# Performance work log

Hardware: AMD Instinct MI355X
Metric: run time of the kernel (lower is better)

The kernel has to match this reference:

```python
import jax, jax.numpy as jnp
import numpy as np
import math

D_MODEL = 1024
N_HEAD = 16


def setup_inputs() -> dict:
    key = jax.random.key(0)
    ks = jax.random.split(key, 11)
    B, S, D = 2, 2048, D_MODEL
    s = 1.0 / math.sqrt(D)
    return {
        "q": jax.random.normal(ks[0], (B, S, D), dtype=jnp.float32),
        "k": jax.random.normal(ks[1], (B, S, D), dtype=jnp.float32),
        "v": jax.random.normal(ks[2], (B, S, D), dtype=jnp.float32),
        "w_q": jax.random.normal(ks[3], (D, D), dtype=jnp.float32) * s,
        "b_q": jnp.zeros((D,), dtype=jnp.float32),
        "w_k": jax.random.normal(ks[4], (D, D), dtype=jnp.float32) * s,
        "b_k": jnp.zeros((D,), dtype=jnp.float32),
        "w_v": jax.random.normal(ks[5], (D, D), dtype=jnp.float32) * s,
        "b_v": jnp.zeros((D,), dtype=jnp.float32),
        "w_out": jax.random.normal(ks[6], (D, D), dtype=jnp.float32) * s,
        "b_out": jnp.zeros((D,), dtype=jnp.float32),
    }


def _split_heads(x, n_head):
    B, S, D = x.shape
    return x.reshape(B, S, n_head, D // n_head).transpose(0, 2, 1, 3)  # [B,H,S,dk]


def reference(q, k, v, w_q, b_q, w_k, b_k, w_v, b_v, w_out, b_out):
    # Linear projections (weights stored as [in, out])
    qh = _split_heads(q @ w_q + b_q, N_HEAD)
    kh = _split_heads(k @ w_k + b_k, N_HEAD)
    vh = _split_heads(v @ w_v + b_v, N_HEAD)
    d_k = qh.shape[-1]
    scores = jnp.einsum("bhqd,bhkd->bhqk", qh, kh) / jnp.sqrt(jnp.float32(d_k))
    attn = jax.nn.softmax(scores, axis=-1)
    context = jnp.einsum("bhqk,bhkd->bhqd", attn, vh)  # [B,H,S,dk]
    B, H, S, dk = context.shape
    context = context.transpose(0, 2, 1, 3).reshape(B, S, H * dk)
    return context @ w_out + b_out
```

## Files before the change

kernel.cpp:

```cpp
#include <hip/hip_runtime.h>
#include <hip/hip_bf16.h>


typedef __bf16 bf16x8 __attribute__((ext_vector_type(8)));
typedef float  f32x4  __attribute__((ext_vector_type(4)));

#define DEVI __device__ __forceinline__
#define SWZ(row, cb) ((cb) ^ (((row) & 7) << 4))

#define GLOAD16(gsrc, ldst)                                                    \
    __builtin_amdgcn_global_load_lds(                                          \
        (const __attribute__((address_space(1))) unsigned int*)(gsrc),         \
        (__attribute__((address_space(3))) unsigned int*)(ldst), 16, 0, 0)

#define BAR()        asm volatile("s_barrier" ::: "memory")
#define WAIT_LGKM0() asm volatile("s_waitcnt lgkmcnt(0)" ::: "memory")
#define WAIT_VM0()   asm volatile("s_waitcnt vmcnt(0)" ::: "memory")
#define WAIT_VM2()   asm volatile("s_waitcnt vmcnt(2)" ::: "memory")

static DEVI unsigned short f2bf(float f) {
    __hip_bfloat16 h = __float2bfloat16(f);
    return __builtin_bit_cast(unsigned short, h);
}
static DEVI unsigned int cvt2(float lo, float hi) {
    unsigned int r;
    asm("v_cvt_pk_bf16_f32 %0, %1, %2" : "=v"(r) : "v"(lo), "v"(hi));
    return r;
}
static DEVI float bf2f(unsigned int lo16) {
    unsigned int x = lo16 << 16;
    return __builtin_bit_cast(float, x);
}
static DEVI bf16x8 ldsRead(const char* p) {
    return __builtin_bit_cast(bf16x8, *(const uint4*)p);
}

__global__ __launch_bounds__(256) void wtrans_kernel(
    const float* w0, const float* w1, const float* w2, const float* w3,
    unsigned short* t0, unsigned short* t1, unsigned short* t2, unsigned short* t3)
{
    __shared__ unsigned short tile[64][80];
    const int z = blockIdx.z;
    const float* w = (z == 0) ? w0 : (z == 1) ? w1 : (z == 2) ? w2 : w3;
    unsigned short* wt = (z == 0) ? t0 : (z == 1) ? t1 : (z == 2) ? t2 : t3;
    const int n0 = blockIdx.x * 64, k0 = blockIdx.y * 64;
    const int t = threadIdx.x;
#pragma unroll
    for (int i = 0; i < 4; i++) {
        int chunk = t + i * 256;
        int row = chunk >> 4, c4 = chunk & 15;
        float4 v = *(const float4*)(w + (size_t)(k0 + row) * 1024 + n0 + c4 * 4);
        tile[c4 * 4 + 0][row] = f2bf(v.x);
        tile[c4 * 4 + 1][row] = f2bf(v.y);
        tile[c4 * 4 + 2][row] = f2bf(v.z);
        tile[c4 * 4 + 3][row] = f2bf(v.w);
    }
    __syncthreads();
#pragma unroll
    for (int i = 0; i < 2; i++) {
        int idx = t + i * 256;
        int row = idx >> 3, ch = idx & 7;
        uint4 vv = *(const uint4*)(&tile[row][ch * 8]);
        *(uint4*)(wt + (size_t)(n0 + row) * 1024 + k0 + ch * 8) = vv;
    }
}

__global__ __launch_bounds__(256, 3) void gemm_proj_kernel(
    const float* x0, const float* x1, const float* x2,
    const unsigned short* wt0, const unsigned short* wt1, const unsigned short* wt2,
    const float* b0, const float* b1, const float* b2,
    unsigned short* y0, unsigned short* y1, unsigned short* y2)
{
    __shared__ __align__(16) char Af[32768];
    __shared__ __align__(16) char Bs[16384];
    const int i = blockIdx.x;
    const int xcd = i & 7, j = i >> 3;
    const int panel = xcd * 12 + (j >> 3);
    const int z = panel >> 5, mblk = panel & 31;
    const int n0 = (j & 7) * 128, m0 = mblk * 128;

    const float* X = (z == 0) ? x0 : (z == 1) ? x1 : x2;
    const unsigned short* Wt = (z == 0) ? wt0 : (z == 1) ? wt1 : wt2;
    const float* bias = (z == 0) ? b0 : (z == 1) ? b1 : b2;
    unsigned short* Y = (z == 0) ? y0 : (z == 1) ? y1 : y2;
    const float scale = (z == 0) ? 0.125f * 1.44269504f : 1.0f;
    const int t = threadIdx.x, w = t >> 6, l = t & 63, l15 = l & 15, l4 = l >> 4;
    const int wr = w >> 1, wc = w & 1;
    const char* Ab = (const char*)X;
    const char* Bb = (const char*)Wt;

    f32x4 acc[4][4];
#pragma unroll
    for (int mr = 0; mr < 4; mr++)
#pragma unroll
        for (int nc = 0; nc < 4; nc++) acc[mr][nc] = f32x4{0.f, 0.f, 0.f, 0.f};

#pragma unroll 1
    for (int k = 0; k < 16; ++k) {
        const int k0 = k * 64;
        BAR();
#pragma unroll
        for (int jj = 0; jj < 8; jj++) {
            int o = w * 8192 + jj * 1024 + l * 16;
            int row = o >> 8, cb = (o >> 4) & 15;
            int csw = cb ^ ((row & 7) << 1);
            GLOAD16(Ab + ((size_t)(m0 + row) * 1024 + k0 + csw * 4) * 4,
                    Af + w * 8192 + jj * 1024);
        }
#pragma unroll
        for (int jj = 0; jj < 4; jj++) {
            int o = w * 4096 + jj * 1024 + l * 16;
            int row = o >> 7, cb = (o >> 4) & 7;
            int csw = cb ^ (row & 7);
            GLOAD16(Bb + ((size_t)(n0 + row) * 1024 + k0 + csw * 8) * 2,
                    Bs + w * 4096 + jj * 1024);
        }
        WAIT_VM0();
        BAR();

        bf16x8 af[4][2], bfr[4][2];
#pragma unroll
        for (int mr = 0; mr < 4; mr++) {
            int row = wr * 64 + mr * 16 + l15;
            int x = (row & 7) << 1;
#pragma unroll
            for (int kf = 0; kf < 2; kf++) {
                int cb = kf * 8 + l4 * 2;
                const char* p = Af + row * 256 + (cb ^ x) * 16;
                float4 a = *(const float4*)p;
                float4 b = *(const float4*)(p + 16);
                uint4 pk = {cvt2(a.x, a.y), cvt2(a.z, a.w),
                            cvt2(b.x, b.y), cvt2(b.z, b.w)};
                af[mr][kf] = __builtin_bit_cast(bf16x8, pk);
            }
        }
#pragma unroll
        for (int nc = 0; nc < 4; nc++) {
            int row = wc * 64 + nc * 16 + l15;
#pragma unroll
            for (int kf = 0; kf < 2; kf++)
                bfr[nc][kf] = ldsRead(Bs + row * 128 + SWZ(row, kf * 64 + l4 * 16));
        }
        __builtin_amdgcn_s_setprio(1);
#pragma unroll
        for (int kf = 0; kf < 2; kf++)
#pragma unroll
            for (int mr = 0; mr < 4; mr++)
#pragma unroll
                for (int nc = 0; nc < 4; nc++)
                    acc[mr][nc] = __builtin_amdgcn_mfma_f32_16x16x32_bf16(
                        af[mr][kf], bfr[nc][kf], acc[mr][nc], 0, 0, 0);
        __builtin_amdgcn_s_setprio(0);
    }

    WAIT_LGKM0();
    BAR();
    char* Es = Af;
    if (z < 2) {
#pragma unroll
        for (int nc = 0; nc < 4; nc++) {
            float bv = bias[n0 + wc * 64 + nc * 16 + l15];
#pragma unroll
            for (int mr = 0; mr < 4; mr++) {
#pragma unroll
                for (int r = 0; r < 2; r++) {
                    int mloc = wr * 64 + mr * 16 + l4 * 4 + r * 2;
                    int nloc = wc * 64 + nc * 16 + l15;
                    unsigned int pk = cvt2((acc[mr][nc][r * 2] + bv) * scale,
                                           (acc[mr][nc][r * 2 + 1] + bv) * scale);
                    *(unsigned short*)(Es + mloc * 256 + nloc * 2) =
                        (unsigned short)(pk & 0xffff);
                    *(unsigned short*)(Es + (mloc + 1) * 256 + nloc * 2) =
                        (unsigned short)(pk >> 16);
                }
            }
        }
        WAIT_LGKM0();
        BAR();
#pragma unroll
        for (int ii = 0; ii < 8; ii++) {
            int idx = t + ii * 256, row = idx >> 4, ch = idx & 15;
            *(uint4*)((char*)Y + ((size_t)(m0 + row) * 1024 + n0 + ch * 8) * 2) =
                *(const uint4*)(Es + row * 256 + ch * 16);
        }
    } else {
#pragma unroll
        for (int nc = 0; nc < 4; nc++) {
            float bv = bias[n0 + wc * 64 + nc * 16 + l15];
#pragma unroll
            for (int mr = 0; mr < 4; mr++) {
#pragma unroll
                for (int r = 0; r < 2; r++) {
                    int mloc = wr * 64 + mr * 16 + l4 * 4 + r * 2;
                    int nloc = wc * 64 + nc * 16 + l15;
                    unsigned int pk = cvt2(acc[mr][nc][r * 2] + bv,
                                           acc[mr][nc][r * 2 + 1] + bv);
                    *(unsigned int*)(Es + nloc * 256 + mloc * 2) = pk;
                }
            }
        }
        WAIT_LGKM0();
        BAR();
        const int bb = m0 >> 11, s0 = m0 & 2047;
#pragma unroll
        for (int ii = 0; ii < 8; ii++) {
            int idx = t + ii * 256, row = idx >> 4, ch = idx & 15;
            int col = n0 + row, h = col >> 6, d = col & 63;
            *(uint4*)((char*)Y +
                      (((size_t)((bb * 16 + h) * 64 + d)) * 2048 + s0 + ch * 8) * 2) =
                *(const uint4*)(Es + row * 256 + ch * 16);
        }
    }
}

__global__ __launch_bounds__(256, 4) void attn_kernel(
    const unsigned short* Q2, const unsigned short* K2, const unsigned short* VT,
    unsigned short* Opart, float* lpart)
{
    __shared__ __align__(16) char sm[40960];
    char* Pall = sm;
    char* K0s = sm + 16384;
    char* K1s = sm + 24576;
    char* Vs  = sm + 32768;
    const int t = threadIdx.x, w = t >> 6, l = t & 63, l15 = l & 15, l4 = l >> 4;
    char* Ps = Pall + w * 4096;

    const int i = blockIdx.x;
    const int xcd = i & 7, j = i >> 3;
    const int bh = xcd * 4 + (j >> 5);
    const int jj = j & 31, qblk = jj >> 1, kh = jj & 1;
    const int b = bh >> 4, h = bh & 15;
    const int q0 = qblk * 128;
    const char* Qb = (const char*)(Q2 + ((size_t)(b * 2048 + q0)) * 1024 + h * 64);
    const char* Kb = (const char*)(K2 + ((size_t)(b * 2048)) * 1024 + h * 64);
    const char* Vb = (const char*)(VT + (size_t)bh * 64 * 2048);

    int kGO[2], vGO[2];
#pragma unroll
    for (int jj2 = 0; jj2 < 2; jj2++) {
        int row = w * 16 + jj2 * 8 + (l >> 3);
        int ch = (l & 7) ^ (row & 7);
        kGO[jj2] = row * 2048 + ch * 16;
        vGO[jj2] = row * 4096 + ch * 16;
    }
    int kRO[4][2];
#pragma unroll
    for (int cc = 0; cc < 4; cc++) {
        int row = cc * 16 + l15;
#pragma unroll
        for (int kf = 0; kf < 2; kf++)
            kRO[cc][kf] = row * 128 + SWZ(row, kf * 64 + l4 * 16);
    }
    int pWO[2][4], pRO[2][2];
#pragma unroll
    for (int qi = 0; qi < 2; qi++) {
        int row = qi * 16 + l15;
#pragma unroll
        for (int cc = 0; cc < 4; cc++) {
            int c = (cc * 2 + (l4 >> 1)) ^ (l15 & 7);
            pWO[qi][cc] = row * 128 + c * 16 + (l4 & 1) * 8;
        }
#pragma unroll
        for (int kf = 0; kf < 2; kf++)
            pRO[qi][kf] = row * 128 + SWZ(row, kf * 64 + l4 * 16);
    }

#define STAGE_K(TT, Kdst)                                                      \
    do {                                                                       \
        int kk0 = (TT) * 64;                                                   \
        _Pragma("unroll") for (int s2 = 0; s2 < 2; s2++)                       \
            GLOAD16(Kb + (size_t)(kk0 * 2048 + kGO[s2]),                       \
                    (Kdst) + w * 2048 + s2 * 1024);                            \
    } while (0)
#define STAGE_V(TT)                                                            \
    do {                                                                       \
        int kk0 = (TT) * 64;                                                   \
        _Pragma("unroll") for (int s2 = 0; s2 < 2; s2++)                       \
            GLOAD16(Vb + (size_t)(kk0 * 2 + vGO[s2]),                          \
                    Vs + w * 2048 + s2 * 1024);                                \
    } while (0)

    bf16x8 qf[2][2];
#pragma unroll
    for (int qi = 0; qi < 2; qi++) {
        int row = w * 32 + qi * 16 + l15;
#pragma unroll
        for (int kf = 0; kf < 2; kf++)
            qf[qi][kf] = __builtin_bit_cast(
                bf16x8, *(const uint4*)(Qb + (size_t)row * 2048 + kf * 64 + l4 * 16));
    }

    const int tbase = kh * 16;
    STAGE_K(tbase + (qblk & 15), K0s);
    STAGE_V(tbase + (qblk & 15));
    WAIT_VM0();
    BAR();

    bf16x8 ones;
#pragma unroll
    for (int e = 0; e < 8; e++) ones[e] = (__bf16)1.0f;

    f32x4 o[2][4], ol[2];
#pragma unroll
    for (int qi = 0; qi < 2; qi++) {
#pragma unroll
        for (int c = 0; c < 4; c++) o[qi][c] = f32x4{0.f, 0.f, 0.f, 0.f};
        ol[qi] = f32x4{0.f, 0.f, 0.f, 0.f};
    }

#pragma unroll 1
    for (int it = 0; it < 16; it++) {
        char* Kc = (it & 1) ? K1s : K0s;
        char* Kn = (it & 1) ? K0s : K1s;
        if (it < 15) STAGE_K(tbase + ((qblk + it + 1) & 15), Kn);

        f32x4 sacc[2][4];
#pragma unroll
        for (int qi = 0; qi < 2; qi++)
#pragma unroll
            for (int c = 0; c < 4; c++) sacc[qi][c] = f32x4{0.f, 0.f, 0.f, 0.f};
        __builtin_amdgcn_s_setprio(1);
#pragma unroll
        for (int cc = 0; cc < 4; cc++)
#pragma unroll
            for (int kf = 0; kf < 2; kf++) {
                bf16x8 kfrag = ldsRead(Kc + kRO[cc][kf]);
#pragma unroll
                for (int qi = 0; qi < 2; qi++)
                    sacc[qi][cc] = __builtin_amdgcn_mfma_f32_16x16x32_bf16(
                        kfrag, qf[qi][kf], sacc[qi][cc], 0, 0, 0);
            }
        __builtin_amdgcn_s_setprio(0);

#pragma unroll
        for (int qi = 0; qi < 2; qi++)
#pragma unroll
            for (int cc = 0; cc < 4; cc++)
#pragma unroll
                for (int r = 0; r < 4; r++)
                    sacc[qi][cc][r] = __builtin_amdgcn_exp2f(sacc[qi][cc][r]);

#pragma unroll
        for (int qi = 0; qi < 2; qi++)
#pragma unroll
            for (int cc = 0; cc < 4; cc++) {
                uint2 pk = {cvt2(sacc[qi][cc][0], sacc[qi][cc][1]),
                            cvt2(sacc[qi][cc][2], sacc[qi][cc][3])};
                *(uint2*)(Ps + pWO[qi][cc]) = pk;
            }
        asm volatile("" ::: "memory");
        bf16x8 pf[2][2];
#pragma unroll
        for (int qi = 0; qi < 2; qi++)
#pragma unroll
            for (int kf = 0; kf < 2; kf++)
                pf[qi][kf] = ldsRead(Ps + pRO[qi][kf]);

        if (it < 15) { WAIT_VM2(); } else { WAIT_VM0(); }
        BAR();

        __builtin_amdgcn_s_setprio(1);
#pragma unroll
        for (int dd = 0; dd < 4; dd++)
#pragma unroll
            for (int kf = 0; kf < 2; kf++) {
                bf16x8 vfrag = ldsRead(Vs + kRO[dd][kf]);
#pragma unroll
                for (int qi = 0; qi < 2; qi++)
                    o[qi][dd] = __builtin_amdgcn_mfma_f32_16x16x32_bf16(
                        vfrag, pf[qi][kf], o[qi][dd], 0, 0, 0);
            }
#pragma unroll
        for (int qi = 0; qi < 2; qi++)
#pragma unroll
            for (int kf = 0; kf < 2; kf++)
                ol[qi] = __builtin_amdgcn_mfma_f32_16x16x32_bf16(
                    ones, pf[qi][kf], ol[qi], 0, 0, 0);
        __builtin_amdgcn_s_setprio(0);

        WAIT_LGKM0();
        BAR();
        if (it < 15) {
            STAGE_V(tbase + ((qblk + it + 1) & 15));
            WAIT_VM2();
            BAR();
        }
    }
#undef STAGE_K
#undef STAGE_V

    const size_t qgbase = (size_t)bh * 2048 + q0 + w * 32;
#pragma unroll
    for (int qi = 0; qi < 2; qi++) {
        size_t qg = qgbase + qi * 16 + l15;
        unsigned short* orow = Opart + ((size_t)kh * 65536 + qg) * 64;
#pragma unroll
        for (int dd = 0; dd < 4; dd++) {
            uint2 pk = {cvt2(o[qi][dd][0], o[qi][dd][1]),
                        cvt2(o[qi][dd][2], o[qi][dd][3])};
            *(uint2*)(orow + dd * 16 + l4 * 4) = pk;
        }
        if (l4 == 0) lpart[(size_t)kh * 65536 + qg] = ol[qi][0];
    }
}

__global__ __launch_bounds__(256) void reduce_kernel(
    const unsigned short* Op, const float* lp, unsigned short* ctx)
{
    int idx = blockIdx.x * 256 + threadIdx.x;
    int qg = idx >> 3, c8 = idx & 7;
    uint4 a = *(const uint4*)(Op + (size_t)qg * 64 + c8 * 8);
    uint4 bq = *(const uint4*)(Op + (size_t)65536 * 64 + (size_t)qg * 64 + c8 * 8);
    float rinv = 1.0f / (lp[qg] + lp[65536 + qg]);
    const unsigned int* pa = (const unsigned int*)&a;
    const unsigned int* pb = (const unsigned int*)&bq;
    unsigned int outp[4];
#pragma unroll
    for (int j = 0; j < 4; j++) {
        float s0 = (bf2f(pa[j] & 0xffff) + bf2f(pb[j] & 0xffff)) * rinv;
        float s1 = (bf2f(pa[j] >> 16) + bf2f(pb[j] >> 16)) * rinv;
        outp[j] = cvt2(s0, s1);
    }
    int bh = qg >> 11, s = qg & 2047, b = bh >> 4, h = bh & 15;
    *(uint4*)(ctx + ((size_t)(b * 2048 + s)) * 1024 + h * 64 + c8 * 8) =
        *(const uint4*)outp;
}

__global__ __launch_bounds__(256, 3) void gemm_out_kernel(
    const unsigned short* ctx, const unsigned short* wto, const float* bias, float* out)
{
    __shared__ __align__(16) char As[16384];
    __shared__ __align__(16) char Bs[16384];
    const int i = blockIdx.x;
    const int xcd = i & 7, j = i >> 3;
    const int mpanel = xcd * 4 + (j >> 3);
    const int n0 = (j & 7) * 128, m0 = mpanel * 128;
    const int t = threadIdx.x, w = t >> 6, l = t & 63, l15 = l & 15, l4 = l >> 4;
    const int wr = w >> 1, wc = w & 1;
    const char* Ab = (const char*)ctx;
    const char* Bb = (const char*)wto;

    f32x4 acc[4][4];
#pragma unroll
    for (int mr = 0; mr < 4; mr++)
#pragma unroll
        for (int nc = 0; nc < 4; nc++) acc[mr][nc] = f32x4{0.f, 0.f, 0.f, 0.f};

#pragma unroll 1
    for (int k = 0; k < 16; ++k) {
        const int k0 = k * 64;
        BAR();
#pragma unroll
        for (int jj = 0; jj < 4; jj++) {
            int o = w * 4096 + jj * 1024 + l * 16;
            int row = o >> 7, cb = (o >> 4) & 7;
            int csw = cb ^ (row & 7);
            GLOAD16(Ab + ((size_t)(m0 + row) * 1024 + k0 + csw * 8) * 2,
                    As + w * 4096 + jj * 1024);
        }
#pragma unroll
        for (int jj = 0; jj < 4; jj++) {
            int o = w * 4096 + jj * 1024 + l * 16;
            int row = o >> 7, cb = (o >> 4) & 7;
            int csw = cb ^ (row & 7);
            GLOAD16(Bb + ((size_t)(n0 + row) * 1024 + k0 + csw * 8) * 2,
                    Bs + w * 4096 + jj * 1024);
        }
        WAIT_VM0();
        BAR();

        bf16x8 af[4][2], bfr[4][2];
#pragma unroll
        for (int mr = 0; mr < 4; mr++) {
            int row = wr * 64 + mr * 16 + l15;
#pragma unroll
            for (int kf = 0; kf < 2; kf++)
                af[mr][kf] = ldsRead(As + row * 128 + SWZ(row, kf * 64 + l4 * 16));
        }
#pragma unroll
        for (int nc = 0; nc < 4; nc++) {
            int row = wc * 64 + nc * 16 + l15;
#pragma unroll
            for (int kf = 0; kf < 2; kf++)
                bfr[nc][kf] = ldsRead(Bs + row * 128 + SWZ(row, kf * 64 + l4 * 16));
        }
        __builtin_amdgcn_s_setprio(1);
#pragma unroll
        for (int kf = 0; kf < 2; kf++)
#pragma unroll
            for (int mr = 0; mr < 4; mr++)
#pragma unroll
                for (int nc = 0; nc < 4; nc++)
                    acc[mr][nc] = __builtin_amdgcn_mfma_f32_16x16x32_bf16(
                        af[mr][kf], bfr[nc][kf], acc[mr][nc], 0, 0, 0);
        __builtin_amdgcn_s_setprio(0);
    }

#pragma unroll
    for (int nc = 0; nc < 4; nc++) {
        int col = n0 + wc * 64 + nc * 16 + l15;
        float bv = bias[col];
#pragma unroll
        for (int mr = 0; mr < 4; mr++)
#pragma unroll
            for (int r = 0; r < 4; r++) {
                int m = m0 + wr * 64 + mr * 16 + l4 * 4 + r;
                out[(size_t)m * 1024 + col] = acc[mr][nc][r] + bv;
            }
    }
}

extern "C" void kernel_launch(void* const* d_in, const int* in_sizes, int n_in,
                              void* d_out, int out_size, void* d_ws, size_t ws_size,
                              hipStream_t stream)
{
    (void)in_sizes; (void)n_in; (void)out_size; (void)ws_size;
    const float* q  = (const float*)d_in[0];
    const float* k  = (const float*)d_in[1];
    const float* v  = (const float*)d_in[2];
    const float* wq = (const float*)d_in[3];
    const float* bq = (const float*)d_in[4];
    const float* wk = (const float*)d_in[5];
    const float* bk = (const float*)d_in[6];
    const float* wv = (const float*)d_in[7];
    const float* bv = (const float*)d_in[8];
    const float* wo = (const float*)d_in[9];
    const float* bo = (const float*)d_in[10];

    char* ws = (char*)d_ws;
    const size_t MB = 1u << 20;
    unsigned short* WTq = (unsigned short*)(ws + 0 * MB);
    unsigned short* WTk = (unsigned short*)(ws + 2 * MB);
    unsigned short* WTv = (unsigned short*)(ws + 4 * MB);
    unsigned short* WTo = (unsigned short*)(ws + 6 * MB);
    unsigned short* Q2  = (unsigned short*)(ws + 8 * MB);
    unsigned short* K2  = (unsigned short*)(ws + 16 * MB);
    unsigned short* VT  = (unsigned short*)(ws + 24 * MB);
    unsigned short* CTX = (unsigned short*)(ws + 32 * MB);
    unsigned short* OPART = (unsigned short*)(ws + 40 * MB);
    float*          LPART = (float*)(ws + 57 * MB);

    wtrans_kernel<<<dim3(16, 16, 4), 256, 0, stream>>>(wq, wk, wv, wo, WTq, WTk, WTv, WTo);
    gemm_proj_kernel<<<768, 256, 0, stream>>>(q, k, v, WTq, WTk, WTv,
                                              bq, bk, bv, Q2, K2, VT);
    attn_kernel<<<1024, 256, 0, stream>>>(Q2, K2, VT, OPART, LPART);
    reduce_kernel<<<2048, 256, 0, stream>>>(OPART, LPART, CTX);
    gemm_out_kernel<<<256, 256, 0, stream>>>(CTX, WTo, bo, (float*)d_out);
}
```

Measured before the change: 117.7 us.

## Double-buffer projection GEMM LDS tiles with K=32 stages and async prefetch

```diff
diff --git a/kernel.cpp b/kernel.cpp
--- a/kernel.cpp
+++ b/kernel.cpp
@@ -17,6 +17,7 @@
 #define WAIT_LGKM0() asm volatile("s_waitcnt lgkmcnt(0)" ::: "memory")
 #define WAIT_VM0()   asm volatile("s_waitcnt vmcnt(0)" ::: "memory")
 #define WAIT_VM2()   asm volatile("s_waitcnt vmcnt(2)" ::: "memory")
+#define WAIT_VM6()   asm volatile("s_waitcnt vmcnt(6)" ::: "memory")
 
 static DEVI unsigned short f2bf(float f) {
     __hip_bfloat16 h = __float2bfloat16(f);
@@ -71,8 +72,11 @@
     const float* b0, const float* b1, const float* b2,
     unsigned short* y0, unsigned short* y1, unsigned short* y2)
 {
-    __shared__ __align__(16) char Af[32768];
-    __shared__ __align__(16) char Bs[16384];
+    __shared__ __align__(16) char sm[49152];
+    char* Afb0 = sm;
+    char* Afb1 = sm + 16384;
+    char* Bsb0 = sm + 32768;
+    char* Bsb1 = sm + 40960;
     const int i = blockIdx.x;
     const int xcd = i & 7, j = i >> 3;
     const int panel = xcd * 12 + (j >> 3);
@@ -89,73 +93,83 @@
     const char* Ab = (const char*)X;
     const char* Bb = (const char*)Wt;
 
+    int aRow[4], aCsw[4];
+#pragma unroll
+    for (int jj = 0; jj < 4; jj++) {
+        int o = w * 4096 + jj * 1024 + l * 16;
+        aRow[jj] = o >> 7;
+        aCsw[jj] = (l & 7) ^ (aRow[jj] & 7);
+    }
+    int bRow[2], bCsw[2];
+#pragma unroll
+    for (int jj = 0; jj < 2; jj++) {
+        int o = w * 2048 + jj * 1024 + l * 16;
+        bRow[jj] = o >> 6;
+        bCsw[jj] = ((o >> 4) & 3) ^ (bRow[jj] & 3);
+    }
+
+#define STAGE(K0, ab, bb_)                                                     \
+    do {                                                                       \
+        _Pragma("unroll") for (int jj = 0; jj < 4; jj++)                       \
+            GLOAD16(Ab + ((size_t)(m0 + aRow[jj]) * 1024 + (K0)) * 4 + aCsw[jj] * 16, \
+                    (ab) + w * 4096 + jj * 1024);                              \
+        _Pragma("unroll") for (int jj = 0; jj < 2; jj++)                       \
+            GLOAD16(Bb + ((size_t)(n0 + bRow[jj]) * 1024 + (K0)) * 2 + bCsw[jj] * 16, \
+                    (bb_) + w * 2048 + jj * 1024);                             \
+    } while (0)
+
     f32x4 acc[4][4];
 #pragma unroll
     for (int mr = 0; mr < 4; mr++)
 #pragma unroll
         for (int nc = 0; nc < 4; nc++) acc[mr][nc] = f32x4{0.f, 0.f, 0.f, 0.f};
 
+    STAGE(0, Afb0, Bsb0);
+
 #pragma unroll 1
-    for (int k = 0; k < 16; ++k) {
-        const int k0 = k * 64;
-        BAR();
-#pragma unroll
-        for (int jj = 0; jj < 8; jj++) {
-            int o = w * 8192 + jj * 1024 + l * 16;
-            int row = o >> 8, cb = (o >> 4) & 15;
-            int csw = cb ^ ((row & 7) << 1);
-            GLOAD16(Ab + ((size_t)(m0 + row) * 1024 + k0 + csw * 4) * 4,
-                    Af + w * 8192 + jj * 1024);
-        }
-#pragma unroll
-        for (int jj = 0; jj < 4; jj++) {
-            int o = w * 4096 + jj * 1024 + l * 16;
-            int row = o >> 7, cb = (o >> 4) & 7;
-            int csw = cb ^ (row & 7);
-            GLOAD16(Bb + ((size_t)(n0 + row) * 1024 + k0 + csw * 8) * 2,
-                    Bs + w * 4096 + jj * 1024);
-        }
-        WAIT_VM0();
-        BAR();
-
-        bf16x8 af[4][2], bfr[4][2];
+    for (int k = 0; k < 32; ++k) {
+        char* Ac = (k & 1) ? Afb1 : Afb0;
+        char* Bc = (k & 1) ? Bsb1 : Bsb0;
+        if (k < 31) {
+            STAGE((k + 1) * 32, (k & 1) ? Afb0 : Afb1, (k & 1) ? Bsb0 : Bsb1);
+            WAIT_VM6();
+        } else {
+            WAIT_VM0();
+        }
+        BAR();
+
+        bf16x8 af[4], bfr[4];
 #pragma unroll
         for (int mr = 0; mr < 4; mr++) {
             int row = wr * 64 + mr * 16 + l15;
-            int x = (row & 7) << 1;
-#pragma unroll
-            for (int kf = 0; kf < 2; kf++) {
-                int cb = kf * 8 + l4 * 2;
-                const char* p = Af + row * 256 + (cb ^ x) * 16;
-                float4 a = *(const float4*)p;
-                float4 b = *(const float4*)(p + 16);
-                uint4 pk = {cvt2(a.x, a.y), cvt2(a.z, a.w),
-                            cvt2(b.x, b.y), cvt2(b.z, b.w)};
-                af[mr][kf] = __builtin_bit_cast(bf16x8, pk);
-            }
+            int x = row & 7;
+            const char* base = Ac + row * 128;
+            float4 a = *(const float4*)(base + (((l4 * 2) ^ x) * 16));
+            float4 b2 = *(const float4*)(base + (((l4 * 2 + 1) ^ x) * 16));
+            uint4 pk = {cvt2(a.x, a.y), cvt2(a.z, a.w),
+                        cvt2(b2.x, b2.y), cvt2(b2.z, b2.w)};
+            af[mr] = __builtin_bit_cast(bf16x8, pk);
         }
 #pragma unroll
         for (int nc = 0; nc < 4; nc++) {
             int row = wc * 64 + nc * 16 + l15;
-#pragma unroll
-            for (int kf = 0; kf < 2; kf++)
-                bfr[nc][kf] = ldsRead(Bs + row * 128 + SWZ(row, kf * 64 + l4 * 16));
+            bfr[nc] = ldsRead(Bc + row * 64 + ((l4 ^ (row & 3)) * 16));
         }
         __builtin_amdgcn_s_setprio(1);
 #pragma unroll
-        for (int kf = 0; kf < 2; kf++)
-#pragma unroll
-            for (int mr = 0; mr < 4; mr++)
-#pragma unroll
-                for (int nc = 0; nc < 4; nc++)
-                    acc[mr][nc] = __builtin_amdgcn_mfma_f32_16x16x32_bf16(
-                        af[mr][kf], bfr[nc][kf], acc[mr][nc], 0, 0, 0);
+        for (int mr = 0; mr < 4; mr++)
+#pragma unroll
+            for (int nc = 0; nc < 4; nc++)
+                acc[mr][nc] = __builtin_amdgcn_mfma_f32_16x16x32_bf16(
+                    af[mr], bfr[nc], acc[mr][nc], 0, 0, 0);
         __builtin_amdgcn_s_setprio(0);
-    }
-
-    WAIT_LGKM0();
-    BAR();
-    char* Es = Af;
+
+        WAIT_LGKM0();
+        BAR();
+    }
+#undef STAGE
+
+    char* Es = sm;
     if (z < 2) {
 #pragma unroll
         for (int nc = 0; nc < 4; nc++) {
```

Measured after the change: 120.7 us. +2.6%, slower.
